# Kernel optimization log

Hardware: AMD Instinct MI355X
Metric: run time of the kernel (lower is better)

Reference implementation:

```python
import jax, jax.numpy as jnp
import numpy as np

B, S, E, H = 4, 1024, 1024, 16
HD = E // H  # head_dim = 64
MAX_SEQ = 1024  # rel positions span [-(MAX_SEQ-1), MAX_SEQ-1]


def setup_inputs() -> dict:
    key = jax.random.key(0)
    ks = jax.random.split(key, 12)
    std_e = 1.0 / np.sqrt(E)
    std_h = 1.0 / np.sqrt(HD)
    inp = {
        "x": jax.random.normal(ks[0], (B, S, E), dtype=jnp.float32),
        # torch nn.Linear weights are [out, in]; y = x @ W.T + b
        "Wq": jax.random.uniform(ks[1], (E, E), jnp.float32, -std_e, std_e),
        "bq": jax.random.uniform(ks[2], (E,), jnp.float32, -std_e, std_e),
        "Wk": jax.random.uniform(ks[3], (E, E), jnp.float32, -std_e, std_e),
        "bk": jax.random.uniform(ks[4], (E,), jnp.float32, -std_e, std_e),
        "Wv": jax.random.uniform(ks[5], (E, E), jnp.float32, -std_e, std_e),
        "bv": jax.random.uniform(ks[6], (E,), jnp.float32, -std_e, std_e),
        "Wo": jax.random.uniform(ks[7], (E, E), jnp.float32, -std_e, std_e),
        "bo": jax.random.uniform(ks[8], (E,), jnp.float32, -std_e, std_e),
        # pos_key_proj: Linear(head_dim, head_dim, bias=False)
        "Wp": jax.random.uniform(ks[9], (HD, HD), jnp.float32, -std_h, std_h),
        # learned relative position table [2*max_seq_len-1, head_dim]
        "rel_table": jax.random.normal(ks[10], (2 * MAX_SEQ - 1, HD), dtype=jnp.float32),
    }
    return inp


def _rel_shift(pos_scores):
    # pos_scores: [B, H, S, 2S-1] -> [B, H, S, S]
    # result[..., i, j] = pos_scores[..., i, (S-1) - i + j]
    s = pos_scores.shape[-2]
    idx = (s - 1) - jnp.arange(s)[:, None] + jnp.arange(s)[None, :]  # [S, S]
    return jnp.take_along_axis(pos_scores, idx[None, None, :, :], axis=-1)


def reference(x, Wq, bq, Wk, bk, Wv, bv, Wo, bo, Wp, rel_table):
    scale = 1.0 / np.sqrt(HD)
    Q = (x @ Wq.T + bq).reshape(B, S, H, HD).transpose(0, 2, 1, 3)  # [B,H,S,HD]
    K = (x @ Wk.T + bk).reshape(B, S, H, HD).transpose(0, 2, 1, 3)
    V = (x @ Wv.T + bv).reshape(B, S, H, HD).transpose(0, 2, 1, 3)

    # rel_pos_encoding(S): slice centered at MAX_SEQ-1 covering 2S-1 positions
    center = MAX_SEQ - 1
    rel_emb = rel_table[center - (S - 1): center + S]  # [2S-1, HD]
    rel_key = rel_emb @ Wp.T                            # [2S-1, HD]

    content = jnp.einsum("bhqd,bhkd->bhqk", Q, K) * scale       # [B,H,S,S]
    pos = jnp.einsum("bhqd,pd->bhqp", Q, rel_key) * scale       # [B,H,S,2S-1]
    scores = content + _rel_shift(pos)                          # [B,H,S,S]

    probs = jax.nn.softmax(scores, axis=-1)
    ctx = jnp.einsum("bhqk,bhkd->bhqd", probs, V)               # [B,H,S,HD]
    ctx = ctx.transpose(0, 2, 1, 3).reshape(B, S, E)
    return ctx @ Wo.T + bo
```

## Files before the change

kernel.cpp:

```cpp
#include <hip/hip_runtime.h>
#include <hip/hip_bf16.h>

#define B_   4
#define S_   1024
#define E_   1024
#define H_   16
#define HD_  64

typedef float  f32x4  __attribute__((ext_vector_type(4)));
typedef short  bf16x8 __attribute__((ext_vector_type(8)));
typedef short  bf16x4 __attribute__((ext_vector_type(4)));

__device__ __forceinline__ float bf2f(short u) {
  union { unsigned int i; float f; } v;
  v.i = ((unsigned int)(unsigned short)u) << 16;
  return v.f;
}
__device__ __forceinline__ short f2bf(float f) {
  unsigned int x = __float_as_uint(f);
  x = x + 0x7fffu + ((x >> 16) & 1u);
  return (short)(x >> 16);
}
__device__ __forceinline__ bf16x8 ld_cvt8(const float* __restrict__ p) {
  const f32x4 a = *(const f32x4*)p;
  const f32x4 b = *(const f32x4*)(p + 4);
  bf16x8 r;
  r[0] = f2bf(a[0]); r[1] = f2bf(a[1]); r[2] = f2bf(a[2]); r[3] = f2bf(a[3]);
  r[4] = f2bf(b[0]); r[5] = f2bf(b[1]); r[6] = f2bf(b[2]); r[7] = f2bf(b[3]);
  return r;
}

__device__ __forceinline__ void gload_lds16(const short* g, short* l) {
  __builtin_amdgcn_global_load_lds(
      (const __attribute__((address_space(1))) void*)g,
      (__attribute__((address_space(3))) void*)l, 16, 0, 0);
}

__global__ __launch_bounds__(256) void prep_kernel(
    const float* __restrict__ w0, const float* __restrict__ w1,
    const float* __restrict__ w2, const float* __restrict__ x,
    const float* __restrict__ wo, const float* __restrict__ rel,
    const float* __restrict__ Wp,
    short* __restrict__ WB, short* __restrict__ xbf,
    short* __restrict__ WoB, short* __restrict__ RKw)
{
  const int NW = E_ * E_;
  const int y  = blockIdx.y;

  if (y == 8) {
    if (blockIdx.x >= 32) return;
    const int tid  = threadIdx.x;
    const int lane = tid & 63;
    const int wv   = tid >> 6;
    const int quad = lane >> 4;
    const int l15  = lane & 15;
    const int p0   = blockIdx.x * 64 + wv * 16;

    bf16x8 af[2];
    {
      int prow = p0 + l15; if (prow > 2046) prow = 2046;
      const float* ap = rel + (size_t)prow * 64 + quad * 8;
      af[0] = ld_cvt8(ap);
      af[1] = ld_cvt8(ap + 32);
    }
    f32x4 acc[4] = {};
#pragma unroll
    for (int nt = 0; nt < 4; ++nt) {
      const float* bp = Wp + (size_t)(nt * 16 + l15) * 64 + quad * 8;
      acc[nt] = __builtin_amdgcn_mfma_f32_16x16x32_bf16(af[0], ld_cvt8(bp),      acc[nt], 0, 0, 0);
      acc[nt] = __builtin_amdgcn_mfma_f32_16x16x32_bf16(af[1], ld_cvt8(bp + 32), acc[nt], 0, 0, 0);
    }
#pragma unroll
    for (int r = 0; r < 4; ++r) {
      const int p = p0 + quad * 4 + r;
      if (p < 2047)
#pragma unroll
        for (int nt = 0; nt < 4; ++nt)
          RKw[(size_t)p * 64 + nt * 16 + l15] = f2bf(acc[nt][r]);
    }
    return;
  }

  const float* src;
  short* dst;
  if (y < 3)      { src = (y == 0) ? w0 : (y == 1) ? w1 : w2; dst = WB + (size_t)y * NW; }
  else if (y < 7) { src = x + (size_t)(y - 3) * NW;           dst = xbf + (size_t)(y - 3) * NW; }
  else            { src = wo;                                  dst = WoB; }
  const int i = (blockIdx.x * 256 + threadIdx.x) * 4;
  const f32x4 v = *(const f32x4*)(src + i);
  bf16x4 o;
  o[0] = f2bf(v[0]); o[1] = f2bf(v[1]); o[2] = f2bf(v[2]); o[3] = f2bf(v[3]);
  *(bf16x4*)(dst + i) = o;
}

__global__ __launch_bounds__(256) void gemm_cat(
    const short* __restrict__ A, const short* __restrict__ W,
    const float* __restrict__ b0, const float* __restrict__ b1, const float* __restrict__ b2,
    short* __restrict__ Qo, short* __restrict__ Ko, short* __restrict__ Vt)
{
  __shared__ short As[128 * 32];
  __shared__ short Bs[128 * 32];

  const int tid  = threadIdx.x;
  const int lane = tid & 63;
  const int wave = tid >> 6;
  const int quad = lane >> 4;
  const int l15  = lane & 15;
  const int wmb  = (wave >> 1) * 64;
  const int wnb  = (wave & 1) * 64;

  const int lid = blockIdx.x;
  const int idx = lid >> 3;
  const int m0  = ((lid & 7) * 4 + (idx & 3)) * 128;
  const int n0  = (idx >> 2) * 128;

  const int trow = tid >> 2;
  const int tc   = tid & 3;

  f32x4 acc[4][4] = {};

  for (int k0 = 0; k0 < E_; k0 += 32) {
#pragma unroll
    for (int n = 0; n < 2; ++n) {
      const int row  = trow + n * 64;
      const int srcc = tc ^ ((row >> 1) & 3);
      gload_lds16(A + (size_t)(m0 + row) * E_ + k0 + srcc * 8, &As[n * 2048 + tid * 8]);
    }
#pragma unroll
    for (int n = 0; n < 2; ++n) {
      const int row  = trow + n * 64;
      const int srcc = tc ^ ((row >> 1) & 3);
      gload_lds16(W + (size_t)(n0 + row) * E_ + k0 + srcc * 8, &Bs[n * 2048 + tid * 8]);
    }
    __syncthreads();

    bf16x8 af[4], bfr[4];
#pragma unroll
    for (int i = 0; i < 4; ++i) {
      const int row = wmb + i * 16 + l15;
      const int pc  = quad ^ ((row >> 1) & 3);
      af[i] = *(bf16x8*)&As[row * 32 + pc * 8];
    }
#pragma unroll
    for (int j = 0; j < 4; ++j) {
      const int row = wnb + j * 16 + l15;
      const int pc  = quad ^ ((row >> 1) & 3);
      bfr[j] = *(bf16x8*)&Bs[row * 32 + pc * 8];
    }
#pragma unroll
    for (int i = 0; i < 4; ++i)
#pragma unroll
      for (int j = 0; j < 4; ++j)
        acc[i][j] = __builtin_amdgcn_mfma_f32_16x16x32_bf16(af[i], bfr[j], acc[i][j], 0, 0, 0);
    __syncthreads();
  }

  const int z = n0 >> 10;
  const float* bz = (z == 0) ? b0 : (z == 1) ? b1 : b2;

  if (z == 2) {
    const int mtb = m0 + wmb;
    const int bq  = mtb >> 10;
    const int kt  = (mtb >> 6) & 15;
#pragma unroll
    for (int j = 0; j < 4; ++j) {
      const int n = n0 + wnb + j * 16 + l15;
      const float bv = bz[n & 1023];
      const int h = (n >> 6) & 15;
      const int d = n & 63;
      bf16x8 lo, hi;
#pragma unroll
      for (int e = 0; e < 8; ++e) {
        lo[e] = f2bf(acc[e & 3][j][e >> 2] + bv);
        hi[e] = f2bf(acc[e & 3][j][(e >> 2) + 2] + bv);
      }
      const size_t off = ((size_t)((bq * 16 + h) * 64 + d)) * 1024 + kt * 64 + quad * 16;
      *(bf16x8*)(Vt + off)     = lo;
      *(bf16x8*)(Vt + off + 8) = hi;
    }
  } else {
    short* C = z ? Ko : Qo;
#pragma unroll
    for (int j = 0; j < 4; ++j) {
      const int n  = n0 + wnb + j * 16 + l15;
      const int nc = n & 1023;
      const float bv = bz[nc];
#pragma unroll
      for (int i = 0; i < 4; ++i) {
        const int m = m0 + wmb + i * 16 + quad * 4;
#pragma unroll
        for (int r = 0; r < 4; ++r)
          C[(size_t)(m + r) * E_ + nc] = f2bf(acc[i][j][r] + bv);
      }
    }
  }
}

__global__ __launch_bounds__(256) void gemm_o(
    const short* __restrict__ A, const short* __restrict__ W,
    const float* __restrict__ bb, float* __restrict__ C)
{
  __shared__ short As[128 * 32];
  __shared__ short Bs[128 * 32];

  const int tid  = threadIdx.x;
  const int lane = tid & 63;
  const int wave = tid >> 6;
  const int quad = lane >> 4;
  const int l15  = lane & 15;
  const int wmb  = (wave >> 1) * 64;
  const int wnb  = (wave & 1) * 64;

  const int lid = blockIdx.x;
  const int idx = lid >> 3;
  const int m0  = ((lid & 7) * 4 + (idx & 3)) * 128;
  const int n0  = (idx >> 2) * 128;

  const int trow = tid >> 2;
  const int tc   = tid & 3;

  f32x4 acc[4][4] = {};

  for (int k0 = 0; k0 < E_; k0 += 32) {
#pragma unroll
    for (int n = 0; n < 2; ++n) {
      const int row  = trow + n * 64;
      const int srcc = tc ^ ((row >> 1) & 3);
      gload_lds16(A + (size_t)(m0 + row) * E_ + k0 + srcc * 8, &As[n * 2048 + tid * 8]);
    }
#pragma unroll
    for (int n = 0; n < 2; ++n) {
      const int row  = trow + n * 64;
      const int srcc = tc ^ ((row >> 1) & 3);
      gload_lds16(W + (size_t)(n0 + row) * E_ + k0 + srcc * 8, &Bs[n * 2048 + tid * 8]);
    }
    __syncthreads();

    bf16x8 af[4], bfr[4];
#pragma unroll
    for (int i = 0; i < 4; ++i) {
      const int row = wmb + i * 16 + l15;
      const int pc  = quad ^ ((row >> 1) & 3);
      af[i] = *(bf16x8*)&As[row * 32 + pc * 8];
    }
#pragma unroll
    for (int j = 0; j < 4; ++j) {
      const int row = wnb + j * 16 + l15;
      const int pc  = quad ^ ((row >> 1) & 3);
      bfr[j] = *(bf16x8*)&Bs[row * 32 + pc * 8];
    }
#pragma unroll
    for (int i = 0; i < 4; ++i)
#pragma unroll
      for (int j = 0; j < 4; ++j)
        acc[i][j] = __builtin_amdgcn_mfma_f32_16x16x32_bf16(af[i], bfr[j], acc[i][j], 0, 0, 0);
    __syncthreads();
  }

#pragma unroll
  for (int j = 0; j < 4; ++j) {
    const int n = n0 + wnb + j * 16 + l15;
    const float bv = bb[n];
#pragma unroll
    for (int i = 0; i < 4; ++i) {
      const int m = m0 + wmb + i * 16 + quad * 4;
#pragma unroll
      for (int r = 0; r < 4; ++r)
        C[(size_t)(m + r) * E_ + n] = acc[i][j][r] + bv;
    }
  }
}

__global__ __launch_bounds__(512, 4) void attn_kernel(
    const short* Qw, const short* __restrict__ Kw,
    const short* __restrict__ Vtg, const short* __restrict__ RKw,
    short* Cw)
{
  __shared__ short Ks[64][72];
  __shared__ short Vt[64][72];
  __shared__ short RKs[256][72];
  __shared__ short Ps[8][16][72];

  const int tid  = threadIdx.x;
  const int lane = tid & 63;
  const int wv   = tid >> 6;
  const int quad = lane >> 4;
  const int l15  = lane & 15;

  const int lid  = blockIdx.x;
  const int pair = (lid & 7) * 8 + (lid >> 6);
  const int qt   = (lid >> 3) & 7;
  const int b    = pair >> 4;
  const int h    = pair & 15;
  const int bh   = pair;
  const int q0   = qt * 128;
  const int qw0  = q0 + wv * 16;
  const int jb   = 112 - 16 * wv;
  const int pbase0 = S_ - 128 - q0;

  bf16x8 qf[2];
  {
    const size_t base = (size_t)(b * S_ + qw0 + l15) * E_ + h * HD_ + quad * 8;
    qf[0] = *(const bf16x8*)(Qw + base);
    qf[1] = *(const bf16x8*)(Qw + base + 32);
  }

  f32x4 oacc[4] = {};
  float lsum[4] = {0.f, 0.f, 0.f, 0.f};

  const float fs = 0.125f * 1.44269504088896340736f;

  const int sr  = tid >> 3;
  const int sc8 = (tid & 7) * 8;

  {
    *(bf16x8*)&Ks[sr][sc8] =
        *(const bf16x8*)(Kw + (size_t)(b * S_ + sr) * E_ + h * HD_ + sc8);
    *(bf16x8*)&Vt[sr][sc8] =
        *(const bf16x8*)(Vtg + (size_t)(bh * 64 + sr) * 1024 + sc8);
#pragma unroll
    for (int jj = 0; jj < 3; ++jj) {
      const int c = tid + jj * 512;
      const int row = c >> 3, ch = (c & 7) * 8;
      int p = pbase0 + row; p = (p > 2046) ? 2046 : p;
      *(bf16x8*)&RKs[row][ch] = *(const bf16x8*)(RKw + (size_t)p * 64 + ch);
    }
    __syncthreads();
  }

#pragma unroll 1
  for (int kt = 0; kt < 16; ++kt) {
    bf16x8 kreg, vreg, rkreg;
    const bool havekv = (kt < 15);
    const bool haverk = (kt < 15);
    if (havekv) {
      kreg = *(const bf16x8*)(Kw + (size_t)(b * S_ + (kt + 1) * 64 + sr) * E_ + h * HD_ + sc8);
      vreg = *(const bf16x8*)(Vtg + (size_t)(bh * 64 + sr) * 1024 + (kt + 1) * 64 + sc8);
    }
    if (haverk) {
      int p = pbase0 + 64 * (kt + 3) + sr; if (p > 2046) p = 2046;
      rkreg = *(const bf16x8*)(RKw + (size_t)p * 64 + sc8);
    }

    f32x4 sc[4] = {};
#pragma unroll
    for (int s = 0; s < 2; ++s) {
#pragma unroll
      for (int kk = 0; kk < 4; ++kk) {
        bf16x8 bf = *(bf16x8*)&Ks[kk*16 + l15][s*32 + quad*8];
        sc[kk] = __builtin_amdgcn_mfma_f32_16x16x32_bf16(qf[s], bf, sc[kk], 0, 0, 0);
      }
    }

    f32x4 ta[5] = {};
#pragma unroll
    for (int jt = 0; jt < 5; ++jt) {
      const int off  = jb + jt * 16;
      const int slot = (kt + (off >> 6)) & 3;
      const int prow = slot * 64 + (off & 63);
#pragma unroll
      for (int s = 0; s < 2; ++s) {
        bf16x8 bf = *(bf16x8*)&RKs[prow + l15][s*32 + quad*8];
        ta[jt] = __builtin_amdgcn_mfma_f32_16x16x32_bf16(qf[s], bf, ta[jt], 0, 0, 0);
      }
    }

    float p[4][4];
#pragma unroll
    for (int r = 0; r < 4; ++r) {
      const int i16 = quad*4 + r;
      const int d   = 15 + l15 - i16;
      const int srcLane = (quad << 4) | (d & 15);
      float sj[5];
#pragma unroll
      for (int jt = 0; jt < 5; ++jt) sj[jt] = __shfl(ta[jt][r], srcLane, 64);
      const bool hi = (d >= 16);
#pragma unroll
      for (int kk = 0; kk < 4; ++kk) {
        const float t = hi ? sj[kk+1] : sj[kk];
        const float sv = fminf((sc[kk][r] + t) * fs, 108.f);
        const float pv = exp2f(sv - 12.f);
        p[kk][r] = pv;
        lsum[r] += pv;
      }
    }

#pragma unroll
    for (int r = 0; r < 4; ++r) {
      bf16x4 pw;
      pw[0] = f2bf(p[0][r]); pw[1] = f2bf(p[1][r]);
      pw[2] = f2bf(p[2][r]); pw[3] = f2bf(p[3][r]);
      *(bf16x4*)&Ps[wv][quad*4 + r][l15*4] = pw;
    }

#pragma unroll
    for (int ks = 0; ks < 2; ++ks) {
      bf16x8 pa = *(bf16x8*)&Ps[wv][l15][ks*32 + quad*8];
#pragma unroll
      for (int dt = 0; dt < 4; ++dt) {
        bf16x8 vb = *(bf16x8*)&Vt[dt*16 + l15][ks*32 + quad*8];
        oacc[dt] = __builtin_amdgcn_mfma_f32_16x16x32_bf16(pa, vb, oacc[dt], 0, 0, 0);
      }
    }

    __syncthreads();
    if (havekv) {
      *(bf16x8*)&Ks[sr][sc8] = kreg;
      *(bf16x8*)&Vt[sr][sc8] = vreg;
    }
    if (haverk) {
      *(bf16x8*)&RKs[((kt + 3) & 3) * 64 + sr][sc8] = rkreg;
    }
    __syncthreads();
  }

#pragma unroll
  for (int off = 1; off <= 8; off <<= 1)
#pragma unroll
    for (int r = 0; r < 4; ++r)
      lsum[r] += __shfl_xor(lsum[r], off, 64);

#pragma unroll
  for (int r = 0; r < 4; ++r) {
    const float inv = 1.0f / lsum[r];
    const size_t row = (size_t)(b * S_ + qw0 + quad*4 + r) * E_ + h * HD_;
#pragma unroll
    for (int dt = 0; dt < 4; ++dt)
      Cw[row + dt*16 + l15] = f2bf(oacc[dt][r] * inv);
  }
}

__global__ void fill_kernel(float* __restrict__ out, int n, float val) {
  for (int i = blockIdx.x * blockDim.x + threadIdx.x; i < n; i += gridDim.x * blockDim.x)
    out[i] = val;
}

extern "C" void kernel_launch(void* const* d_in, const int* in_sizes, int n_in,
                              void* d_out, int out_size, void* d_ws, size_t ws_size,
                              hipStream_t stream)
{
  const size_t WS_NEEDED = 33816448;
  if (ws_size < WS_NEEDED) {
    fill_kernel<<<1024, 256, 0, stream>>>((float*)d_out, out_size, 0.25f);
    return;
  }
  if (n_in != 11 || in_sizes[10] != 2047 * 64) {
    fill_kernel<<<1024, 256, 0, stream>>>((float*)d_out, out_size, 0.75f);
    return;
  }

  const float* x   = (const float*)d_in[0];
  const float* Wq  = (const float*)d_in[1];
  const float* bq  = (const float*)d_in[2];
  const float* Wk  = (const float*)d_in[3];
  const float* bk  = (const float*)d_in[4];
  const float* Wv  = (const float*)d_in[5];
  const float* bv  = (const float*)d_in[6];
  const float* Wo  = (const float*)d_in[7];
  const float* bo  = (const float*)d_in[8];
  const float* Wp  = (const float*)d_in[9];
  const float* rel = (const float*)d_in[10];

  char* ws = (char*)d_ws;
  short* Qws = (short*)(ws);
  short* Kws = (short*)(ws + 8388608);
  short* Vtg = (short*)(ws + 16777216);
  short* WB  = (short*)(ws + 25165824);
  short* WoB = (short*)(ws + 31457280);
  short* RKw = (short*)(ws + 33554432);
  short* xbf = (short*)d_out;

  prep_kernel<<<dim3(1024, 9), dim3(256), 0, stream>>>(
      Wq, Wk, Wv, x, Wo, rel, Wp, WB, xbf, WoB, RKw);

  gemm_cat<<<dim3(768), dim3(256), 0, stream>>>(
      xbf, WB, bq, bk, bv, Qws, Kws, Vtg);

  attn_kernel<<<dim3(512), dim3(512), 0, stream>>>(Qws, Kws, Vtg, RKw, Qws);

  gemm_o<<<dim3(256), dim3(256), 0, stream>>>(Qws, WoB, bo, (float*)d_out);
}
```

Baseline: 249.0 us.

## Double-buffer output projection GEMM with smaller 64x128 tiles and more blocks

Rewrites the output projection GEMM to use 64x128 tiles (512 blocks instead of 256) so more blocks are available to fill the 256 CUs. It also double-buffers the LDS stages so the next K-slice's global-to-LDS load is issued before computing on the current one, which removes one barrier per iteration. The trade-off is lower per-block data reuse, since each wave now computes a 64x32 output.

```diff
diff --git a/kernel.cpp b/kernel.cpp
--- a/kernel.cpp
+++ b/kernel.cpp
@@ -196,74 +196,78 @@
   }
 }
 
-__global__ __launch_bounds__(256) void gemm_o(
+__global__ __launch_bounds__(256) void gemm_out(
     const short* __restrict__ A, const short* __restrict__ W,
     const float* __restrict__ bb, float* __restrict__ C)
 {
-  __shared__ short As[128 * 32];
-  __shared__ short Bs[128 * 32];
+  __shared__ short As[2][64 * 32];
+  __shared__ short Bs[2][128 * 32];
 
   const int tid  = threadIdx.x;
   const int lane = tid & 63;
   const int wave = tid >> 6;
   const int quad = lane >> 4;
   const int l15  = lane & 15;
-  const int wmb  = (wave >> 1) * 64;
-  const int wnb  = (wave & 1) * 64;
+  const int wnb  = wave * 32;
 
   const int lid = blockIdx.x;
-  const int idx = lid >> 3;
-  const int m0  = ((lid & 7) * 4 + (idx & 3)) * 128;
-  const int n0  = (idx >> 2) * 128;
+  const int m0  = ((lid & 7) * 8 + ((lid >> 3) & 7)) * 64;
+  const int n0  = (lid >> 6) * 128;
 
   const int trow = tid >> 2;
   const int tc   = tid & 3;
 
-  f32x4 acc[4][4] = {};
-
-  for (int k0 = 0; k0 < E_; k0 += 32) {
+  auto stage = [&](int k0, int bsel) {
+    {
+      const int srcc = tc ^ ((trow >> 1) & 3);
+      gload_lds16(A + (size_t)(m0 + trow) * E_ + k0 + srcc * 8, &As[bsel][tid * 8]);
+    }
 #pragma unroll
     for (int n = 0; n < 2; ++n) {
       const int row  = trow + n * 64;
       const int srcc = tc ^ ((row >> 1) & 3);
-      gload_lds16(A + (size_t)(m0 + row) * E_ + k0 + srcc * 8, &As[n * 2048 + tid * 8]);
-    }
-#pragma unroll
-    for (int n = 0; n < 2; ++n) {
-      const int row  = trow + n * 64;
-      const int srcc = tc ^ ((row >> 1) & 3);
-      gload_lds16(W + (size_t)(n0 + row) * E_ + k0 + srcc * 8, &Bs[n * 2048 + tid * 8]);
-    }
-    __syncthreads();
-
-    bf16x8 af[4], bfr[4];
+      gload_lds16(W + (size_t)(n0 + row) * E_ + k0 + srcc * 8, &Bs[bsel][n * 2048 + tid * 8]);
+    }
+  };
+
+  f32x4 acc[4][2] = {};
+
+  stage(0, 0);
+  __syncthreads();
+
+#pragma unroll 2
+  for (int t = 0; t < 32; ++t) {
+    const int cur = t & 1;
+    if (t < 31) stage((t + 1) * 32, cur ^ 1);
+
+    bf16x8 af[4], bfr[2];
 #pragma unroll
     for (int i = 0; i < 4; ++i) {
-      const int row = wmb + i * 16 + l15;
+      const int row = i * 16 + l15;
       const int pc  = quad ^ ((row >> 1) & 3);
-      af[i] = *(bf16x8*)&As[row * 32 + pc * 8];
-    }
-#pragma unroll
-    for (int j = 0; j < 4; ++j) {
+      af[i] = *(bf16x8*)&As[cur][row * 32 + pc * 8];
+    }
+#pragma unroll
+    for (int j = 0; j < 2; ++j) {
       const int row = wnb + j * 16 + l15;
       const int pc  = quad ^ ((row >> 1) & 3);
-      bfr[j] = *(bf16x8*)&Bs[row * 32 + pc * 8];
+      bfr[j] = *(bf16x8*)&Bs[cur][row * 32 + pc * 8];
     }
 #pragma unroll
     for (int i = 0; i < 4; ++i)
 #pragma unroll
-      for (int j = 0; j < 4; ++j)
+      for (int j = 0; j < 2; ++j)
         acc[i][j] = __builtin_amdgcn_mfma_f32_16x16x32_bf16(af[i], bfr[j], acc[i][j], 0, 0, 0);
     __syncthreads();
   }
 
 #pragma unroll
-  for (int j = 0; j < 4; ++j) {
+  for (int j = 0; j < 2; ++j) {
     const int n = n0 + wnb + j * 16 + l15;
     const float bv = bb[n];
 #pragma unroll
     for (int i = 0; i < 4; ++i) {
-      const int m = m0 + wmb + i * 16 + quad * 4;
+      const int m = m0 + i * 16 + quad * 4;
 #pragma unroll
       for (int r = 0; r < 4; ++r)
         C[(size_t)(m + r) * E_ + n] = acc[i][j][r] + bv;
@@ -478,5 +482,5 @@
 
   attn_kernel<<<dim3(512), dim3(512), 0, stream>>>(Qws, Kws, Vtg, RKw, Qws);
 
-  gemm_o<<<dim3(256), dim3(256), 0, stream>>>(Qws, WoB, bo, (float*)d_out);
-}
+  gemm_out<<<dim3(512), dim3(256), 0, stream>>>(Qws, WoB, bo, (float*)d_out);
+}
```

After: 246.9 us. No clear change (-0.9%).
